# Kernel optimization log

Hardware: AMD Instinct MI355X
Metric: run time of the kernel (lower is better)

## Reference

```python
import math
import jax, jax.numpy as jnp
import numpy as np

PI_APPROX = 3.1415926  # the module's hard-coded pi in KVal


def _factratio(N, D):
    # python-float replica of PRT.factratio
    if N >= D:
        p = 1.0
        for i in range(D + 1, N + 1):
            p *= i
        return p
    p = 1.0
    for i in range(N + 1, D + 1):
        p *= i
    return 1.0 / p


def _kval(M, L):
    return math.sqrt((2 * L + 1) / (4 * PI_APPROX) * _factratio(L - M, L + M))


def _assoc_legendre(M, L, x):
    # x = cos(theta), |x| <= 1 by construction so the zero-guard branch never fires
    pmm = jnp.ones_like(x)
    if M > 0:
        somx2 = jnp.sqrt((1.0 + x) * (1.0 - x))
        fact = 1.0
        for _ in range(1, M + 1):
            pmm = -pmm * fact * somx2
            fact = fact + 2
    if L == M:
        return pmm
    pmmp1 = x * (2 * M + 1) * pmm
    if L == M + 1:
        return pmmp1
    pll = pmmp1
    for i in range(M + 2, L + 1):
        pll = (x * (2 * i - 1) * pmmp1 - (i + M - 1) * pmm) / (i - M)
        pmm, pmmp1 = pmmp1, pll
    return pll


def _spherical_harmonic(M, L, theta, phi):
    sqrt2 = math.sqrt(2.0)
    ct = jnp.cos(theta)
    if M > 0:
        return sqrt2 * _kval(M, L) * jnp.cos(M * phi) * _assoc_legendre(M, L, ct)
    elif M < 0:
        return sqrt2 * _kval(-M, L) * jnp.sin(-M * phi) * _assoc_legendre(-M, L, ct)
    else:
        return _kval(0, L) * _assoc_legendre(0, L, ct)


def _sh_coeffs(order, phi, theta):
    # [N_rays, S, (order+1)^2] -- loop is over the small fixed harmonic index set
    shs = [_spherical_harmonic(m, l, theta, phi)
           for l in range(order + 1) for m in range(-l, l + 1)]
    return jnp.stack(shs, axis=-1)


def setup_inputs() -> dict:
    key = jax.random.key(0)
    k1, k2, k3 = jax.random.split(key, 3)
    N_RAYS, N, ORDER = 32768, 16, 3
    S = N * N
    xv = jax.random.uniform(k1, (N_RAYS, S), dtype=jnp.float32)
    yv = jax.random.uniform(k2, (N_RAYS, S), dtype=jnp.float32)
    theta = jnp.arccos(1.0 - 2.0 * xv)          # matches sampleSphericalDirections_N_rays
    phi = (2.0 * math.pi) * yv
    # binary visibility per sphere sample
    p_vis = (jax.random.uniform(k3, (N_RAYS, S, 1), dtype=jnp.float32) > 0.5).astype(jnp.float32)
    return {"p_vis": p_vis, "phi": phi, "theta": theta, "n": N, "order": ORDER}


def reference(p_vis, phi, theta, n, order):
    sh = _sh_coeffs(order, phi, theta)           # [R, S, K]
    w = 4.0 * math.pi / (n * n)                   # module uses math.pi here
    prt = jnp.sum(sh * p_vis, axis=1)             # [R, K]
    return jnp.clip(prt * w, -2.0, 2.0)
```

## Files before the change

### kernel.cpp

```cpp
#include <hip/hip_runtime.h>
#include <math.h>


__global__ __launch_bounds__(256) void prt_kernel(
    const float* __restrict__ vis,
    const float* __restrict__ phi,
    const float* __restrict__ theta,
    const int* __restrict__ n_ptr,
    float* __restrict__ out,
    int n_rays)
{
    const int lane = threadIdx.x & 63;
    const int wave = threadIdx.x >> 6;
    const int ray  = blockIdx.x * 4 + wave;
    if (ray >= n_rays) return;

    const int base = ray * 256 + lane * 4;

    const float4 ph = *reinterpret_cast<const float4*>(phi + base);
    const float4 th = *reinterpret_cast<const float4*>(theta + base);
    const float4 vv = *reinterpret_cast<const float4*>(vis + base);

    const float* phs = reinterpret_cast<const float*>(&ph);
    const float* ths = reinterpret_cast<const float*>(&th);
    const float* vvs = reinterpret_cast<const float*>(&vv);

    float acc[16];
    #pragma unroll
    for (int i = 0; i < 16; ++i) acc[i] = 0.0f;

    #pragma unroll
    for (int j = 0; j < 4; ++j) {
        float s, x;
        __sincosf(ths[j], &s, &x);
        float sp, cp;
        __sincosf(phs[j], &sp, &cp);

        const float sq = s * s;
        const float s2 = 2.0f * sp * cp;
        const float c2 = fmaf(-2.0f * sp, sp, 1.0f);
        const float s3 = fmaf(s2, cp, c2 * sp);
        const float c3 = fmaf(-s2, sp, c2 * cp);

        const float v    = vvs[j];
        const float t1   = v * s;
        const float vx   = v * x;
        const float t2   = vx * s;
        const float vsq  = v * sq;
        const float vxsq = vx * sq;
        const float vsqs = vsq * s;

        const float x2  = x * x;
        const float P20 = fmaf(1.5f, x2, -0.5f);
        const float q1  = fmaf(5.0f, x2, -1.0f);
        const float r30 = fmaf(2.5f, x2, -1.5f);
        const float t1q = t1 * q1;

        acc[0]  += v;
        acc[1]   = fmaf(t1,   sp,  acc[1]);
        acc[2]  += vx;
        acc[3]   = fmaf(t1,   cp,  acc[3]);
        acc[4]   = fmaf(vsq,  s2,  acc[4]);
        acc[5]   = fmaf(t2,   sp,  acc[5]);
        acc[6]   = fmaf(v,    P20, acc[6]);
        acc[7]   = fmaf(t2,   cp,  acc[7]);
        acc[8]   = fmaf(vsq,  c2,  acc[8]);
        acc[9]   = fmaf(vsqs, s3,  acc[9]);
        acc[10]  = fmaf(vxsq, s2,  acc[10]);
        acc[11]  = fmaf(t1q,  sp,  acc[11]);
        acc[12]  = fmaf(vx,   r30, acc[12]);
        acc[13]  = fmaf(t1q,  cp,  acc[13]);
        acc[14]  = fmaf(vxsq, c2,  acc[14]);
        acc[15]  = fmaf(vsqs, c3,  acc[15]);
    }

    const bool b0 = (lane & 1) != 0;
    const bool b1 = (lane & 2) != 0;
    const bool b2 = (lane & 4) != 0;
    const bool b3 = (lane & 8) != 0;

    #pragma unroll
    for (int j = 0; j < 8; ++j) {
        const float a0 = acc[2 * j], a1 = acc[2 * j + 1];
        const float keep = b0 ? a1 : a0;
        const float give = b0 ? a0 : a1;
        acc[j] = keep + __shfl_xor(give, 1, 64);
    }
    #pragma unroll
    for (int j = 0; j < 4; ++j) {
        const float a0 = acc[2 * j], a1 = acc[2 * j + 1];
        const float keep = b1 ? a1 : a0;
        const float give = b1 ? a0 : a1;
        acc[j] = keep + __shfl_xor(give, 2, 64);
    }
    #pragma unroll
    for (int j = 0; j < 2; ++j) {
        const float a0 = acc[2 * j], a1 = acc[2 * j + 1];
        const float keep = b2 ? a1 : a0;
        const float give = b2 ? a0 : a1;
        acc[j] = keep + __shfl_xor(give, 4, 64);
    }
    float r;
    {
        const float keep = b3 ? acc[1] : acc[0];
        const float give = b3 ? acc[0] : acc[1];
        r = keep + __shfl_xor(give, 8, 64);
    }
    r += __shfl_xor(r, 16, 64);
    r += __shfl_xor(r, 32, 64);

    const float k01   = b0 ? -0.48860253f : 0.28209481f;
    const float k23   = b0 ? -0.48860253f : 0.48860253f;
    const float k45   = b0 ? -1.09254847f : 0.54627424f;
    const float k67   = b0 ? -1.09254847f : 0.63078316f;
    const float k89   = b0 ? -0.59004360f : 0.54627424f;
    const float k1011 = b0 ? -0.45704580f : 1.44530571f;
    const float k1213 = b0 ? -0.45704580f : 0.74635269f;
    const float k1415 = b0 ? -0.59004360f : 1.44530571f;
    const float ka = b1 ? k23 : k01;
    const float kb = b1 ? k67 : k45;
    const float kc = b1 ? k1011 : k89;
    const float kd = b1 ? k1415 : k1213;
    const float ke = b2 ? kb : ka;
    const float kf = b2 ? kd : kc;
    const float K  = b3 ? kf : ke;

    const int n = *n_ptr;
    const float w = 12.566370614359172f / (float)(n * n);

    const float res = fminf(fmaxf(r * K * w, -2.0f), 2.0f);

    if (lane < 16)
        out[ray * 16 + lane] = res;
}

extern "C" void kernel_launch(void* const* d_in, const int* in_sizes, int n_in,
                              void* d_out, int out_size, void* d_ws, size_t ws_size,
                              hipStream_t stream) {
    const float* vis   = (const float*)d_in[0];
    const float* phi   = (const float*)d_in[1];
    const float* theta = (const float*)d_in[2];
    const int*   n_ptr = (const int*)d_in[3];

    float* out = (float*)d_out;

    const int n_rays = in_sizes[1] / 256;
    const int blocks = (n_rays + 3) / 4;
    prt_kernel<<<blocks, 256, 0, stream>>>(vis, phi, theta, n_ptr, out, n_rays);
}
```

Before: 119.9 us.

## Process four rays per wavefront with 16-lane groups and full-wave output stores

Each wavefront now handles four rays: every 16-lane group owns one ray and loads 16 samples per lane as four float4 loads per input. This drops the last two cross-lane shuffle steps because the butterfly reduction ends within each 16-lane group, and all 64 lanes write outputs instead of 16. The grid shrinks fourfold. The cost is more registers held in flight and fewer waves to hide latency, and there is no per-ray bounds check for a partial final group.

Result: no change. 119.3 us (-0.4%).

```diff
diff --git a/kernel.cpp b/kernel.cpp
--- a/kernel.cpp
+++ b/kernel.cpp
@@ -11,19 +11,22 @@
     int n_rays)
 {
     const int lane = threadIdx.x & 63;
-    const int wave = threadIdx.x >> 6;
-    const int ray  = blockIdx.x * 4 + wave;
-    if (ray >= n_rays) return;
+    const int gwv  = (blockIdx.x * 256 + threadIdx.x) >> 6;
+    const int ray0 = gwv * 4;
+    if (ray0 >= n_rays) return;
 
-    const int base = ray * 256 + lane * 4;
+    const int g = lane >> 4;
+    const int t = lane & 15;
+    const int sbase = (ray0 + g) * 256 + t * 4;
 
-    const float4 ph = *reinterpret_cast<const float4*>(phi + base);
-    const float4 th = *reinterpret_cast<const float4*>(theta + base);
-    const float4 vv = *reinterpret_cast<const float4*>(vis + base);
-
-    const float* phs = reinterpret_cast<const float*>(&ph);
-    const float* ths = reinterpret_cast<const float*>(&th);
-    const float* vvs = reinterpret_cast<const float*>(&vv);
+    float4 ph[4], th[4], vv[4];
+    #pragma unroll
+    for (int j = 0; j < 4; ++j) {
+        const int a = sbase + 64 * j;
+        ph[j] = *reinterpret_cast<const float4*>(phi + a);
+        th[j] = *reinterpret_cast<const float4*>(theta + a);
+        vv[j] = *reinterpret_cast<const float4*>(vis + a);
+    }
 
     float acc[16];
     #pragma unroll
@@ -31,47 +34,53 @@
 
     #pragma unroll
     for (int j = 0; j < 4; ++j) {
-        float s, x;
-        __sincosf(ths[j], &s, &x);
-        float sp, cp;
-        __sincosf(phs[j], &sp, &cp);
+        const float* phs = reinterpret_cast<const float*>(&ph[j]);
+        const float* ths = reinterpret_cast<const float*>(&th[j]);
+        const float* vvs = reinterpret_cast<const float*>(&vv[j]);
+        #pragma unroll
+        for (int e = 0; e < 4; ++e) {
+            float s, x;
+            __sincosf(ths[e], &s, &x);
+            float sp, cp;
+            __sincosf(phs[e], &sp, &cp);
 
-        const float sq = s * s;
-        const float s2 = 2.0f * sp * cp;
-        const float c2 = fmaf(-2.0f * sp, sp, 1.0f);
-        const float s3 = fmaf(s2, cp, c2 * sp);
-        const float c3 = fmaf(-s2, sp, c2 * cp);
+            const float sq = s * s;
+            const float s2 = 2.0f * sp * cp;
+            const float c2 = fmaf(-2.0f * sp, sp, 1.0f);
+            const float s3 = fmaf(s2, cp, c2 * sp);
+            const float c3 = fmaf(-s2, sp, c2 * cp);
 
-        const float v    = vvs[j];
-        const float t1   = v * s;
-        const float vx   = v * x;
-        const float t2   = vx * s;
-        const float vsq  = v * sq;
-        const float vxsq = vx * sq;
-        const float vsqs = vsq * s;
+            const float v    = vvs[e];
+            const float t1   = v * s;
+            const float vx   = v * x;
+            const float t2   = vx * s;
+            const float vsq  = v * sq;
+            const float vxsq = vx * sq;
+            const float vsqs = vsq * s;
 
-        const float x2  = x * x;
-        const float P20 = fmaf(1.5f, x2, -0.5f);
-        const float q1  = fmaf(5.0f, x2, -1.0f);
-        const float r30 = fmaf(2.5f, x2, -1.5f);
-        const float t1q = t1 * q1;
+            const float x2  = x * x;
+            const float P20 = fmaf(1.5f, x2, -0.5f);
+            const float q1  = fmaf(5.0f, x2, -1.0f);
+            const float r30 = fmaf(2.5f, x2, -1.5f);
+            const float t1q = t1 * q1;
 
-        acc[0]  += v;
-        acc[1]   = fmaf(t1,   sp,  acc[1]);
-        acc[2]  += vx;
-        acc[3]   = fmaf(t1,   cp,  acc[3]);
-        acc[4]   = fmaf(vsq,  s2,  acc[4]);
-        acc[5]   = fmaf(t2,   sp,  acc[5]);
-        acc[6]   = fmaf(v,    P20, acc[6]);
-        acc[7]   = fmaf(t2,   cp,  acc[7]);
-        acc[8]   = fmaf(vsq,  c2,  acc[8]);
-        acc[9]   = fmaf(vsqs, s3,  acc[9]);
-        acc[10]  = fmaf(vxsq, s2,  acc[10]);
-        acc[11]  = fmaf(t1q,  sp,  acc[11]);
-        acc[12]  = fmaf(vx,   r30, acc[12]);
-        acc[13]  = fmaf(t1q,  cp,  acc[13]);
-        acc[14]  = fmaf(vxsq, c2,  acc[14]);
-        acc[15]  = fmaf(vsqs, c3,  acc[15]);
+            acc[0]  += v;
+            acc[1]   = fmaf(t1,   sp,  acc[1]);
+            acc[2]  += vx;
+            acc[3]   = fmaf(t1,   cp,  acc[3]);
+            acc[4]   = fmaf(vsq,  s2,  acc[4]);
+            acc[5]   = fmaf(t2,   sp,  acc[5]);
+            acc[6]   = fmaf(v,    P20, acc[6]);
+            acc[7]   = fmaf(t2,   cp,  acc[7]);
+            acc[8]   = fmaf(vsq,  c2,  acc[8]);
+            acc[9]   = fmaf(vsqs, s3,  acc[9]);
+            acc[10]  = fmaf(vxsq, s2,  acc[10]);
+            acc[11]  = fmaf(t1q,  sp,  acc[11]);
+            acc[12]  = fmaf(vx,   r30, acc[12]);
+            acc[13]  = fmaf(t1q,  cp,  acc[13]);
+            acc[14]  = fmaf(vxsq, c2,  acc[14]);
+            acc[15]  = fmaf(vsqs, c3,  acc[15]);
+        }
     }
 
     const bool b0 = (lane & 1) != 0;
@@ -106,8 +115,6 @@
         const float give = b3 ? acc[0] : acc[1];
         r = keep + __shfl_xor(give, 8, 64);
     }
-    r += __shfl_xor(r, 16, 64);
-    r += __shfl_xor(r, 32, 64);
 
     const float k01   = b0 ? -0.48860253f : 0.28209481f;
     const float k23   = b0 ? -0.48860253f : 0.48860253f;
@@ -130,8 +137,7 @@
 
     const float res = fminf(fmaxf(r * K * w, -2.0f), 2.0f);
 
-    if (lane < 16)
-        out[ray * 16 + lane] = res;
+    out[ray0 * 16 + lane] = res;
 }
 
 extern "C" void kernel_launch(void* const* d_in, const int* in_sizes, int n_in,
@@ -145,6 +151,7 @@
     float* out = (float*)d_out;
 
     const int n_rays = in_sizes[1] / 256;
-    const int blocks = (n_rays + 3) / 4;
+    const int rays_per_block = 16;
+    const int blocks = (n_rays + rays_per_block - 1) / rays_per_block;
     prt_kernel<<<blocks, 256, 0, stream>>>(vis, phi, theta, n_ptr, out, n_rays);
 }
```
